# Performance work log

Hardware: AMD Instinct MI355X
Metric: run time of the kernel (lower is better)

## Reference

```python
import jax, jax.numpy as jnp
import numpy as np
from jax import lax

DN = ('NCH', 'OIH', 'NCH')

def _conv(x, w, b, pad):
    # x: [B, C, L]; replication (edge) pad then VALID conv, per nn.ReplicationPad1d + Conv1d
    if pad != (0, 0):
        x = jnp.pad(x, ((0, 0), (0, 0), pad), mode='edge')
    y = lax.conv_general_dilated(x, w, (1,), 'VALID', dimension_numbers=DN)
    return y + b[None, :, None]

def setup_inputs() -> dict:
    key = jax.random.key(0)
    ks = jax.random.split(key, 11)
    B, L, C, H = 32, 512, 300, 512
    s = 1.0 / np.sqrt(C)
    inp = {
        'x': jax.random.normal(ks[0], (B, L, C), jnp.float32),
        'w1': jax.random.normal(ks[1], (C, C, 1), jnp.float32) * s,
        'b1': jax.random.normal(ks[2], (C,), jnp.float32) * s,
        'w2': jax.random.normal(ks[3], (C, C, 2), jnp.float32) * s,
        'b2': jax.random.normal(ks[4], (C,), jnp.float32) * s,
        'w3': jax.random.normal(ks[5], (C, C, 3), jnp.float32) * s,
        'b3': jax.random.normal(ks[6], (C,), jnp.float32) * s,
        'w7': jax.random.normal(ks[7], (C, C, 7), jnp.float32) * s,
        'b7': jax.random.normal(ks[8], (C,), jnp.float32) * s,
        'slp_w': jax.random.normal(ks[9], (H, 5 * C), jnp.float32) * (1.0 / np.sqrt(5 * C)),
        'slp_b': jax.random.normal(ks[10], (H,), jnp.float32) * (1.0 / np.sqrt(5 * C)),
    }
    return inp

def reference(x, w1, b1, w2, b2, w3, b3, w7, b7, slp_w, slp_b):
    xc = jnp.transpose(x, (0, 2, 1))  # [B, C, L]
    x1 = jnp.tanh(_conv(xc, w1, b1, (0, 0)))
    x2 = jnp.tanh(_conv(xc, w2, b2, (0, 1)))
    x3 = jnp.tanh(_conv(xc, w3, b3, (1, 1)))
    x5 = x3  # faithful to the original bug: x5 = self.conv3(x)
    x7 = jnp.tanh(_conv(xc, w7, b7, (3, 3)))
    # concat channels -> [B, L, 1500], then linear + tanh -> [B, L, 512]
    h = jnp.concatenate([x1, x2, x3, x5, x7], axis=1)  # [B, 5C, L]
    h = jnp.transpose(h, (0, 2, 1))  # [B, L, 5C]
    out = jnp.tanh(jnp.einsum('blc,hc->blh', h, slp_w) + slp_b)
    return out
```

## Files before the change

kernel.cpp:

```cpp
#include <hip/hip_runtime.h>
#include <hip/hip_bf16.h>


typedef __attribute__((ext_vector_type(8))) short short8;
typedef __attribute__((ext_vector_type(16))) float floatx16;

#define Bn 32
#define Ln 512
#define Cn 300
#define Hn 512
#define Nn (Bn*Ln)
#define XBP 518
#define XBC 320
#define HK 1216
#define LDSTC 72

#define XROWS 134
#define XSZ (XROWS*LDSTC)
#define HSROWS 128
#define HSSZ (HSROWS*LDSTC)

#define XB_ELEMS (Bn*XBP*XBC)
#define WB_ELEMS 1597440
#define WC_ELEMS (Hn*HK)
#define XB_OFF 0
#define WB_OFF (XB_OFF + XB_ELEMS)
#define WC_OFF (WB_OFF + WB_ELEMS)
#define HB_OFF (WC_OFF + WC_ELEMS)

__device__ __forceinline__ float fast_tanh(float x) {
    float ax = __builtin_fabsf(x);
    float t  = __expf(-2.f * ax);
    float r  = __builtin_fmaf(-2.f * t, __frcp_rn(1.f + t), 1.f);
    return __builtin_copysignf(r, x);
}

__device__ __forceinline__ short f2bf(float v) {
    __hip_bfloat16 h = __float2bfloat16(v);
    return *reinterpret_cast<short*>(&h);
}

__global__ void prep_all(const float* __restrict__ x,
                         const float* __restrict__ w1, const float* __restrict__ w2,
                         const float* __restrict__ w3, const float* __restrict__ w7,
                         const float* __restrict__ slp_w,
                         __hip_bfloat16* __restrict__ wsb) {
    int g = blockIdx.x * 256 + threadIdx.x;
    int idx = g * 8;
    short8 o;
    if (idx < XB_ELEMS) {
        int c8 = idx % XBC;
        int t  = idx / XBC;
        int p = t % XBP;
        int b = t / XBP;
        int l = p - 3;
        l = l < 0 ? 0 : (l > Ln - 1 ? Ln - 1 : l);
        const float* row = x + (b * Ln + l) * Cn;
        if (c8 + 8 <= Cn) {
            float4 a = *(const float4*)(row + c8);
            float4 bq = *(const float4*)(row + c8 + 4);
            o[0] = f2bf(a.x); o[1] = f2bf(a.y); o[2] = f2bf(a.z); o[3] = f2bf(a.w);
            o[4] = f2bf(bq.x); o[5] = f2bf(bq.y); o[6] = f2bf(bq.z); o[7] = f2bf(bq.w);
        } else {
#pragma unroll
            for (int e = 0; e < 8; ++e) {
                int c = c8 + e;
                o[e] = f2bf(c < Cn ? row[c] : 0.f);
            }
        }
        *(short8*)&wsb[idx] = o;
    } else if (idx < WB_OFF + WB_ELEMS) {
        int r = idx - WB_OFF, taps; const float* w;
        if (r < 122880)       { taps = 1; w = w1; }
        else if (r < 368640)  { taps = 2; w = w2; r -= 122880; }
        else if (r < 737280)  { taps = 3; w = w3; r -= 368640; }
        else                  { taps = 7; w = w7; r -= 737280; }
        int lane = (r >> 3) & 63;
        int f    = (r >> 9) & 15;
        int rt   = r >> 13;
        int t    = rt % taps;
        int mc   = rt / taps;
        int ch   = mc % 5;
        int mt   = mc / 5;
        int ks = f >> 2, mq = f & 3;
        int m = mt * 128 + mq * 32 + (lane & 31);
        int cb = ch * 64 + ks * 16 + (lane >> 5) * 8;
#pragma unroll
        for (int e = 0; e < 8; ++e) {
            int c = cb + e;
            o[e] = f2bf((m < Cn && c < Cn) ? w[(m * Cn + c) * taps + t] : 0.f);
        }
        *(short8*)&wsb[idx] = o;
    } else if (idx < WC_OFF + WC_ELEMS) {
        int r = idx - WC_OFF;
        int lane = (r >> 3) & 63;
        int f    = (r >> 9) & 15;
        int mc   = r >> 13;
        int ch   = mc % 19;
        int mt4  = mc / 19;
        int ks = f >> 2, mq = f & 3;
        int h = mt4 * 128 + mq * 32 + (lane & 31);
        int kb = ch * 64 + ks * 16 + (lane >> 5) * 8;
        const float* row = slp_w + h * 1500;
#pragma unroll
        for (int e = 0; e < 8; ++e) {
            int k = kb + e;
            float v;
            if (k < 600)       v = row[k];
            else if (k < 900)  v = row[k] + row[k + 300];
            else if (k < 1200) v = row[k + 300];
            else               v = 0.f;
            o[e] = f2bf(v);
        }
        *(short8*)&wsb[idx] = o;
    }
}

#define MFMA __builtin_amdgcn_mfma_f32_32x32x16_bf16

template<int TAPS, int LEAD>
__device__ __forceinline__ void conv_body(
        const short* __restrict__ xbs, const short* __restrict__ wsp,
        const float* __restrict__ bias, int cid, int mt, int nt,
        __hip_bfloat16* __restrict__ hbuf, short* xs) {
    const int tid  = threadIdx.x;
    const int lane = tid & 63;
    const int wave = tid >> 6;
    const int wn = wave & 1, wm = wave >> 1;
    const int lr = lane & 31;
    const int lk = (lane >> 5) << 3;
    const int TRIG = (TAPS >= 3) ? TAPS - 2 : 0;

    floatx16 acc[2][2];
#pragma unroll
    for (int i = 0; i < 2; i++)
#pragma unroll
        for (int j = 0; j < 2; j++)
#pragma unroll
            for (int r = 0; r < 16; r++) acc[i][j][r] = 0.f;

    short8 bA[8], bB[8], st[5];

#pragma unroll
    for (int i = 0; i < 5; ++i) {
        int j = tid + 256 * i;
        if (i < 4 || j < 1072)
            st[i] = *(const short8*)&xbs[(j >> 3) * XBC + ((j & 7) << 3)];
    }
#pragma unroll
    for (int ks = 0; ks < 4; ++ks)
#pragma unroll
        for (int mf = 0; mf < 2; ++mf)
            bA[ks * 2 + mf] = *(const short8*)&wsp[(ks * 4 + wm * 2 + mf) * 512 + lane * 8];
#pragma unroll
    for (int i = 0; i < 5; ++i) {
        int j = tid + 256 * i;
        if (i < 4 || j < 1072)
            *(short8*)&xs[(j >> 3) * LDSTC + ((j & 7) << 3)] = st[i];
    }
    __syncthreads();

    for (int c5 = 0; c5 < 5; ++c5) {
        const short* cur = xs + (c5 & 1) * XSZ;
        short* nxt = xs + ((c5 + 1) & 1) * XSZ;
        const int c0n = (c5 + 1) * 64;
#pragma unroll
        for (int t = 0; t < TAPS; ++t) {
            if (!(c5 == 4 && t == TAPS - 1)) {
                const short* wtn = (t + 1 < TAPS) ? wsp + (c5 * TAPS + t + 1) * 8192
                                                  : wsp + ((c5 + 1) * TAPS) * 8192;
#pragma unroll
                for (int ks = 0; ks < 4; ++ks)
#pragma unroll
                    for (int mf = 0; mf < 2; ++mf)
                        bB[ks * 2 + mf] = *(const short8*)&wtn[(ks * 4 + wm * 2 + mf) * 512 + lane * 8];
            }
            if (t == TRIG && c5 < 4) {
#pragma unroll
                for (int i = 0; i < 5; ++i) {
                    int j = tid + 256 * i;
                    if (i < 4 || j < 1072)
                        st[i] = *(const short8*)&xbs[(j >> 3) * XBC + c0n + ((j & 7) << 3)];
                }
            }
            const int sh = t - LEAD + 3;
            const int ar = (wn * 64 + lr + sh) * LDSTC + lk;
#pragma unroll
            for (int ks = 0; ks < 4; ++ks) {
                short8 a0 = *(const short8*)&cur[ar + ks * 16];
                short8 a1 = *(const short8*)&cur[ar + 32 * LDSTC + ks * 16];
                acc[0][0] = MFMA(a0, bA[ks * 2 + 0], acc[0][0], 0, 0, 0);
                acc[0][1] = MFMA(a0, bA[ks * 2 + 1], acc[0][1], 0, 0, 0);
                acc[1][0] = MFMA(a1, bA[ks * 2 + 0], acc[1][0], 0, 0, 0);
                acc[1][1] = MFMA(a1, bA[ks * 2 + 1], acc[1][1], 0, 0, 0);
            }
            if (!(c5 == 4 && t == TAPS - 1)) {
#pragma unroll
                for (int f = 0; f < 8; ++f) bA[f] = bB[f];
            }
        }
        if (c5 < 4) {
#pragma unroll
            for (int i = 0; i < 5; ++i) {
                int j = tid + 256 * i;
                if (i < 4 || j < 1072)
                    *(short8*)&nxt[(j >> 3) * LDSTC + ((j & 7) << 3)] = st[i];
            }
        }
        __syncthreads();
    }

#pragma unroll
    for (int mi = 0; mi < 2; ++mi) {
        int mloc = mt * 128 + wm * 64 + mi * 32 + lr;
        int col = cid * Cn + mloc;
        if (mloc < Cn) {
            float bv = bias[mloc];
#pragma unroll
            for (int ni = 0; ni < 2; ++ni) {
                floatx16 v = acc[ni][mi];
#pragma unroll
                for (int reg = 0; reg < 16; ++reg) {
                    int nl = wn * 64 + ni * 32 + (reg & 3) + ((reg >> 2) << 3) + ((lane >> 5) << 2);
                    int n = nt * 128 + nl;
                    hbuf[n * HK + col] = __float2bfloat16(fast_tanh(v[reg] + bv));
                }
            }
        } else if (cid == 3 && col < HK) {
            __hip_bfloat16 z = __float2bfloat16(0.f);
#pragma unroll
            for (int ni = 0; ni < 2; ++ni)
#pragma unroll
                for (int reg = 0; reg < 16; ++reg) {
                    int nl = wn * 64 + ni * 32 + (reg & 3) + ((reg >> 2) << 3) + ((lane >> 5) << 2);
                    int n = nt * 128 + nl;
                    hbuf[n * HK + col] = z;
                }
        }
    }
}

__global__ __launch_bounds__(256, 2) void conv_kernel(
        const __hip_bfloat16* __restrict__ xbg, const __hip_bfloat16* __restrict__ Wbg,
        const float* __restrict__ bias1, const float* __restrict__ bias2,
        const float* __restrict__ bias3, const float* __restrict__ bias7,
        __hip_bfloat16* __restrict__ hbuf) {
    __shared__ __align__(16) short xs[2 * XSZ];

    const int nt = blockIdx.x;
    const int my = blockIdx.y;
    const int g  = my / 3;
    const int mt = my % 3;

    const int b  = nt >> 2;
    const int l0 = (nt & 3) << 7;
    const short* xbs = (const short*)xbg + (b * XBP + l0) * XBC;
    const short* wb  = (const short*)Wbg;

    if (g == 0)      conv_body<7, 3>(xbs, wb + 737280 + mt * 7 * 40960, bias7, 3, mt, nt, hbuf, xs);
    else if (g == 1) conv_body<3, 1>(xbs, wb + 368640 + mt * 3 * 40960, bias3, 2, mt, nt, hbuf, xs);
    else if (g == 2) conv_body<2, 0>(xbs, wb + 122880 + mt * 2 * 40960, bias2, 1, mt, nt, hbuf, xs);
    else             conv_body<1, 0>(xbs, wb +      0 + mt * 1 * 40960, bias1, 0, mt, nt, hbuf, xs);
}

__global__ __launch_bounds__(256, 2) void linear_kernel(
        const __hip_bfloat16* __restrict__ hbufg, const __hip_bfloat16* __restrict__ Wcg,
        const float* __restrict__ slp_b, float* __restrict__ out) {
    __shared__ __align__(16) short hs[2 * HSSZ];

    const int tid  = threadIdx.x;
    const int lane = tid & 63;
    const int wave = tid >> 6;
    const int wn = wave & 1, wm = wave >> 1;
    const int lr = lane & 31;
    const int lk = (lane >> 5) << 3;

    const int nt  = blockIdx.x;
    const int mt4 = blockIdx.y;

    const short* hbp = (const short*)hbufg + nt * 128 * HK;
    const short* wcp = (const short*)Wcg + mt4 * 155648;

    floatx16 acc[2][2];
#pragma unroll
    for (int i = 0; i < 2; i++)
#pragma unroll
        for (int j = 0; j < 2; j++)
#pragma unroll
            for (int r = 0; r < 16; r++) acc[i][j][r] = 0.f;

    short8 bA[8], bB[8], st[4];

#pragma unroll
    for (int i = 0; i < 4; ++i) {
        int j = tid + 256 * i;
        st[i] = *(const short8*)&hbp[(j >> 3) * HK + ((j & 7) << 3)];
    }
#pragma unroll
    for (int ks = 0; ks < 4; ++ks)
#pragma unroll
        for (int mf = 0; mf < 2; ++mf)
            bA[ks * 2 + mf] = *(const short8*)&wcp[(ks * 4 + wm * 2 + mf) * 512 + lane * 8];
#pragma unroll
    for (int i = 0; i < 4; ++i) {
        int j = tid + 256 * i;
        *(short8*)&hs[(j >> 3) * LDSTC + ((j & 7) << 3)] = st[i];
    }
    __syncthreads();

    for (int ch = 0; ch < 19; ++ch) {
        const short* cur = hs + (ch & 1) * HSSZ;
        short* nxt = hs + ((ch + 1) & 1) * HSSZ;
        if (ch < 18) {
            const short* wtn = wcp + (ch + 1) * 8192;
#pragma unroll
            for (int ks = 0; ks < 4; ++ks)
#pragma unroll
                for (int mf = 0; mf < 2; ++mf)
                    bB[ks * 2 + mf] = *(const short8*)&wtn[(ks * 4 + wm * 2 + mf) * 512 + lane * 8];
            const int c0n = (ch + 1) * 64;
#pragma unroll
            for (int i = 0; i < 4; ++i) {
                int j = tid + 256 * i;
                st[i] = *(const short8*)&hbp[(j >> 3) * HK + c0n + ((j & 7) << 3)];
            }
        }
        const int ar = (wn * 64 + lr) * LDSTC + lk;
#pragma unroll
        for (int ks = 0; ks < 4; ++ks) {
            short8 a0 = *(const short8*)&cur[ar + ks * 16];
            short8 a1 = *(const short8*)&cur[ar + 32 * LDSTC + ks * 16];
            acc[0][0] = MFMA(a0, bA[ks * 2 + 0], acc[0][0], 0, 0, 0);
            acc[0][1] = MFMA(a0, bA[ks * 2 + 1], acc[0][1], 0, 0, 0);
            acc[1][0] = MFMA(a1, bA[ks * 2 + 0], acc[1][0], 0, 0, 0);
            acc[1][1] = MFMA(a1, bA[ks * 2 + 1], acc[1][1], 0, 0, 0);
        }
        if (ch < 18) {
#pragma unroll
            for (int f = 0; f < 8; ++f) bA[f] = bB[f];
#pragma unroll
            for (int i = 0; i < 4; ++i) {
                int j = tid + 256 * i;
                *(short8*)&nxt[(j >> 3) * LDSTC + ((j & 7) << 3)] = st[i];
            }
        }
        __syncthreads();
    }

#pragma unroll
    for (int mi = 0; mi < 2; ++mi) {
        int h = mt4 * 128 + wm * 64 + mi * 32 + lr;
        float bv = slp_b[h];
#pragma unroll
        for (int ni = 0; ni < 2; ++ni) {
            floatx16 v = acc[ni][mi];
#pragma unroll
            for (int reg = 0; reg < 16; ++reg) {
                int nl = wn * 64 + ni * 32 + (reg & 3) + ((reg >> 2) << 3) + ((lane >> 5) << 2);
                int n = nt * 128 + nl;
                out[n * Hn + h] = fast_tanh(v[reg] + bv);
            }
        }
    }
}


extern "C" void kernel_launch(void* const* d_in, const int* in_sizes, int n_in,
                              void* d_out, int out_size, void* d_ws, size_t ws_size,
                              hipStream_t stream) {
    const float* x     = (const float*)d_in[0];
    const float* w1    = (const float*)d_in[1];
    const float* b1    = (const float*)d_in[2];
    const float* w2    = (const float*)d_in[3];
    const float* b2    = (const float*)d_in[4];
    const float* w3    = (const float*)d_in[5];
    const float* b3    = (const float*)d_in[6];
    const float* w7    = (const float*)d_in[7];
    const float* b7    = (const float*)d_in[8];
    const float* slp_w = (const float*)d_in[9];
    const float* slp_b = (const float*)d_in[10];

    __hip_bfloat16* wsb = (__hip_bfloat16*)d_ws;

    const int prep_groups = (XB_ELEMS + WB_ELEMS + WC_ELEMS) / 8;
    prep_all<<<(prep_groups + 255) / 256, 256, 0, stream>>>(x, w1, w2, w3, w7, slp_w, wsb);

    conv_kernel<<<dim3(128, 12), 256, 0, stream>>>(wsb + XB_OFF, wsb + WB_OFF,
                                                   b1, b2, b3, b7, wsb + HB_OFF);
    linear_kernel<<<dim3(128, 4), 256, 0, stream>>>(wsb + HB_OFF, wsb + WC_OFF,
                                                    slp_b, (float*)d_out);
}
```

Measured before the change: 191.6 us.

## Process channel chunks in pairs with four LDS buffers, halving barriers

The conv body now keeps four shared-memory input tiles instead of two. It processes two 64-channel chunks per barrier interval and prefetches the next two chunks into registers during the second chunk. This cuts the number of __syncthreads from five to three per block and lengthens the load latency window. The cost is double the LDS footprint (about 77KB per block) and ten staging registers instead of five, which may lower occupancy below the two blocks per CU requested in launch bounds.

```diff
diff --git a/kernel.cpp b/kernel.cpp
--- a/kernel.cpp
+++ b/kernel.cpp
@@ -1,6 +1,5 @@
 #include <hip/hip_runtime.h>
 #include <hip/hip_bf16.h>
-
 
 typedef __attribute__((ext_vector_type(8))) short short8;
 typedef __attribute__((ext_vector_type(16))) float floatx16;
@@ -139,13 +138,15 @@
 #pragma unroll
             for (int r = 0; r < 16; r++) acc[i][j][r] = 0.f;
 
-    short8 bA[8], bB[8], st[5];
+    short8 bA[8], bB[8], st[10];
 
 #pragma unroll
     for (int i = 0; i < 5; ++i) {
         int j = tid + 256 * i;
-        if (i < 4 || j < 1072)
-            st[i] = *(const short8*)&xbs[(j >> 3) * XBC + ((j & 7) << 3)];
+        if (i < 4 || j < 1072) {
+            st[i]     = *(const short8*)&xbs[(j >> 3) * XBC + ((j & 7) << 3)];
+            st[5 + i] = *(const short8*)&xbs[(j >> 3) * XBC + 64 + ((j & 7) << 3)];
+        }
     }
 #pragma unroll
     for (int ks = 0; ks < 4; ++ks)
@@ -155,33 +156,117 @@
 #pragma unroll
     for (int i = 0; i < 5; ++i) {
         int j = tid + 256 * i;
-        if (i < 4 || j < 1072)
-            *(short8*)&xs[(j >> 3) * LDSTC + ((j & 7) << 3)] = st[i];
+        if (i < 4 || j < 1072) {
+            *(short8*)&xs[0 * XSZ + (j >> 3) * LDSTC + ((j & 7) << 3)] = st[i];
+            *(short8*)&xs[1 * XSZ + (j >> 3) * LDSTC + ((j & 7) << 3)] = st[5 + i];
+        }
     }
     __syncthreads();
 
-    for (int c5 = 0; c5 < 5; ++c5) {
-        const short* cur = xs + (c5 & 1) * XSZ;
-        short* nxt = xs + ((c5 + 1) & 1) * XSZ;
-        const int c0n = (c5 + 1) * 64;
-#pragma unroll
-        for (int t = 0; t < TAPS; ++t) {
-            if (!(c5 == 4 && t == TAPS - 1)) {
-                const short* wtn = (t + 1 < TAPS) ? wsp + (c5 * TAPS + t + 1) * 8192
-                                                  : wsp + ((c5 + 1) * TAPS) * 8192;
+    for (int s = 0; s < 2; ++s) {
+        const int cA = 2 * s;
+        const int cB = cA + 1;
+        {
+            const short* cur = xs + (cA & 3) * XSZ;
+#pragma unroll
+            for (int t = 0; t < TAPS; ++t) {
+                const short* wtn = (t + 1 < TAPS) ? wsp + (cA * TAPS + t + 1) * 8192
+                                                  : wsp + ((cA + 1) * TAPS) * 8192;
 #pragma unroll
                 for (int ks = 0; ks < 4; ++ks)
 #pragma unroll
                     for (int mf = 0; mf < 2; ++mf)
                         bB[ks * 2 + mf] = *(const short8*)&wtn[(ks * 4 + wm * 2 + mf) * 512 + lane * 8];
-            }
-            if (t == TRIG && c5 < 4) {
+                const int sh = t - LEAD + 3;
+                const int ar = (wn * 64 + lr + sh) * LDSTC + lk;
+#pragma unroll
+                for (int ks = 0; ks < 4; ++ks) {
+                    short8 a0 = *(const short8*)&cur[ar + ks * 16];
+                    short8 a1 = *(const short8*)&cur[ar + 32 * LDSTC + ks * 16];
+                    acc[0][0] = MFMA(a0, bA[ks * 2 + 0], acc[0][0], 0, 0, 0);
+                    acc[0][1] = MFMA(a0, bA[ks * 2 + 1], acc[0][1], 0, 0, 0);
+                    acc[1][0] = MFMA(a1, bA[ks * 2 + 0], acc[1][0], 0, 0, 0);
+                    acc[1][1] = MFMA(a1, bA[ks * 2 + 1], acc[1][1], 0, 0, 0);
+                }
+#pragma unroll
+                for (int f = 0; f < 8; ++f) bA[f] = bB[f];
+            }
+        }
+        {
+            const short* cur = xs + (cB & 3) * XSZ;
+#pragma unroll
+            for (int t = 0; t < TAPS; ++t) {
+                const short* wtn = (t + 1 < TAPS) ? wsp + (cB * TAPS + t + 1) * 8192
+                                                  : wsp + ((cB + 1) * TAPS) * 8192;
+#pragma unroll
+                for (int ks = 0; ks < 4; ++ks)
+#pragma unroll
+                    for (int mf = 0; mf < 2; ++mf)
+                        bB[ks * 2 + mf] = *(const short8*)&wtn[(ks * 4 + wm * 2 + mf) * 512 + lane * 8];
+                if (t == TRIG) {
+                    const int c0a = (cA + 2) * 64;
+#pragma unroll
+                    for (int i = 0; i < 5; ++i) {
+                        int j = tid + 256 * i;
+                        if (i < 4 || j < 1072)
+                            st[i] = *(const short8*)&xbs[(j >> 3) * XBC + c0a + ((j & 7) << 3)];
+                    }
+                    if (s == 0) {
+#pragma unroll
+                        for (int i = 0; i < 5; ++i) {
+                            int j = tid + 256 * i;
+                            if (i < 4 || j < 1072)
+                                st[5 + i] = *(const short8*)&xbs[(j >> 3) * XBC + 192 + ((j & 7) << 3)];
+                        }
+                    }
+                }
+                const int sh = t - LEAD + 3;
+                const int ar = (wn * 64 + lr + sh) * LDSTC + lk;
+#pragma unroll
+                for (int ks = 0; ks < 4; ++ks) {
+                    short8 a0 = *(const short8*)&cur[ar + ks * 16];
+                    short8 a1 = *(const short8*)&cur[ar + 32 * LDSTC + ks * 16];
+                    acc[0][0] = MFMA(a0, bA[ks * 2 + 0], acc[0][0], 0, 0, 0);
+                    acc[0][1] = MFMA(a0, bA[ks * 2 + 1], acc[0][1], 0, 0, 0);
+                    acc[1][0] = MFMA(a1, bA[ks * 2 + 0], acc[1][0], 0, 0, 0);
+                    acc[1][1] = MFMA(a1, bA[ks * 2 + 1], acc[1][1], 0, 0, 0);
+                }
+#pragma unroll
+                for (int f = 0; f < 8; ++f) bA[f] = bB[f];
+            }
+        }
+        {
+            short* nxtA = xs + ((cA + 2) & 3) * XSZ;
+#pragma unroll
+            for (int i = 0; i < 5; ++i) {
+                int j = tid + 256 * i;
+                if (i < 4 || j < 1072)
+                    *(short8*)&nxtA[(j >> 3) * LDSTC + ((j & 7) << 3)] = st[i];
+            }
+            if (s == 0) {
+                short* nxtB = xs + 3 * XSZ;
 #pragma unroll
                 for (int i = 0; i < 5; ++i) {
                     int j = tid + 256 * i;
                     if (i < 4 || j < 1072)
-                        st[i] = *(const short8*)&xbs[(j >> 3) * XBC + c0n + ((j & 7) << 3)];
-                }
+                        *(short8*)&nxtB[(j >> 3) * LDSTC + ((j & 7) << 3)] = st[5 + i];
+                }
+            }
+        }
+        __syncthreads();
+    }
+
+    {
+        const short* cur = xs;
+#pragma unroll
+        for (int t = 0; t < TAPS; ++t) {
+            if (t + 1 < TAPS) {
+                const short* wtn = wsp + (4 * TAPS + t + 1) * 8192;
+#pragma unroll
+                for (int ks = 0; ks < 4; ++ks)
+#pragma unroll
+                    for (int mf = 0; mf < 2; ++mf)
+                        bB[ks * 2 + mf] = *(const short8*)&wtn[(ks * 4 + wm * 2 + mf) * 512 + lane * 8];
             }
             const int sh = t - LEAD + 3;
             const int ar = (wn * 64 + lr + sh) * LDSTC + lk;
@@ -194,20 +279,11 @@
                 acc[1][0] = MFMA(a1, bA[ks * 2 + 0], acc[1][0], 0, 0, 0);
                 acc[1][1] = MFMA(a1, bA[ks * 2 + 1], acc[1][1], 0, 0, 0);
             }
-            if (!(c5 == 4 && t == TAPS - 1)) {
+            if (t + 1 < TAPS) {
 #pragma unroll
                 for (int f = 0; f < 8; ++f) bA[f] = bB[f];
             }
         }
-        if (c5 < 4) {
-#pragma unroll
-            for (int i = 0; i < 5; ++i) {
-                int j = tid + 256 * i;
-                if (i < 4 || j < 1072)
-                    *(short8*)&nxt[(j >> 3) * LDSTC + ((j & 7) << 3)] = st[i];
-            }
-        }
-        __syncthreads();
     }
 
 #pragma unroll
@@ -245,7 +321,7 @@
         const float* __restrict__ bias1, const float* __restrict__ bias2,
         const float* __restrict__ bias3, const float* __restrict__ bias7,
         __hip_bfloat16* __restrict__ hbuf) {
-    __shared__ __align__(16) short xs[2 * XSZ];
+    __shared__ __align__(16) short xs[4 * XSZ];
 
     const int nt = blockIdx.x;
     const int my = blockIdx.y;
```

After: 200.8 us. 4.8% more time.
